# Kernel tuning notes

Hardware: AMD Instinct MI355X
Metric: run time of the kernel (lower is better)

## Reference

```python
import jax, jax.numpy as jnp
import numpy as np

B, S, E, H = 2, 2048, 2048, 16
D = E // H  # head_dim = 128


def rotate_half(x):
    x1, x2 = jnp.split(x, 2, axis=-1)
    return jnp.concatenate([-x2, x1], axis=-1)


def rope_sincos(seq_len, dim):
    inv_freq = 1.0 / (10000.0 ** (jnp.arange(0, dim, 2, dtype=jnp.float32) / dim))
    t = jnp.arange(seq_len, dtype=jnp.float32)
    freqs = jnp.outer(t, inv_freq)            # [S, D/2]
    emb = jnp.concatenate([freqs, freqs], -1)  # [S, D]
    return jnp.sin(emb), jnp.cos(emb)


def apply_rope(x, sin, cos):
    # x: [B, S, H, D]; sin/cos: [S, D] -> [1, S, 1, D]
    sin = sin[None, :, None, :]
    cos = cos[None, :, None, :]
    return x * cos + rotate_half(x) * sin


def setup_inputs() -> dict:
    key = jax.random.key(0)
    k1, k2 = jax.random.split(key)
    x = jax.random.normal(k1, (B, S, E), dtype=jnp.float32)
    # causal boolean mask [B, 1, S, S]
    mask = jnp.broadcast_to(jnp.tril(jnp.ones((S, S), dtype=bool))[None, None], (B, 1, S, S))
    # fused QKV projection weight (hk.Linear, no bias): [E, 3E]
    W_qkv = jax.random.normal(k2, (E, 3 * E), dtype=jnp.float32) / np.sqrt(E)
    return {"x": x, "mask": mask, "W_qkv": W_qkv}


def reference(x, mask, W_qkv):
    seq_len = x.shape[1]
    qkv = x @ W_qkv                               # [B, S, 3E]
    q, k, v = jnp.split(qkv, 3, axis=-1)
    q = q.reshape(-1, seq_len, H, D)
    k = k.reshape(-1, seq_len, H, D)
    v = v.reshape(-1, seq_len, H, D)
    sin, cos = rope_sincos(seq_len, D)
    q = apply_rope(q, sin, cos)
    k = apply_rope(k, sin, cos)
    attn = jnp.einsum('bqhd,bkhd->bhqk', q, k) / jnp.sqrt(jnp.float32(D))
    m = jnp.broadcast_to(mask, (mask.shape[0], H, seq_len, k.shape[1]))
    attn = jnp.where(m, attn, -jnp.inf)
    attn = jax.nn.softmax(attn, axis=-1)
    out = jnp.einsum('bhqk,bkhd->bqhd', attn, v)
    return out.reshape(-1, seq_len, H * D)
```

## Files before the change

kernel.cpp:

```cpp
#include <hip/hip_runtime.h>

typedef __bf16 bf16;
typedef __bf16 bf16x8 __attribute__((ext_vector_type(8)));
typedef __bf16 bf16x4 __attribute__((ext_vector_type(4)));
typedef float f32x4 __attribute__((ext_vector_type(4)));

#define MFMA16(a, b, c) __builtin_amdgcn_mfma_f32_16x16x32_bf16(a, b, c, 0, 0, 0)

#define Bq 2
#define Sq 2048
#define Eq 2048
#define Hq 16
#define Dq 128
#define N3E 6144

#define GLOAD_LDS16(gp, lp) \
  __builtin_amdgcn_global_load_lds( \
      (const __attribute__((address_space(1))) void*)(gp), \
      (__attribute__((address_space(3))) void*)(lp), 16, 0, 0)

__device__ __forceinline__ bf16 f2bf(float f) {
  unsigned u = __builtin_bit_cast(unsigned, f);
  u += 0x7FFFu + ((u >> 16) & 1u);
  unsigned short h = (unsigned short)(u >> 16);
  return __builtin_bit_cast(bf16, h);
}
__device__ __forceinline__ float bf2f(bf16 b) {
  unsigned short h = __builtin_bit_cast(unsigned short, b);
  return __builtin_bit_cast(float, (unsigned)h << 16);
}

__global__ __launch_bounds__(256) void convert_x(const float* __restrict__ x,
                                                 bf16* __restrict__ xb) {
  const size_t i = ((size_t)blockIdx.x * 256 + threadIdx.x) * 8;
  float4 a = *(const float4*)(x + i);
  float4 b = *(const float4*)(x + i + 4);
  bf16x8 o;
  o[0] = f2bf(a.x); o[1] = f2bf(a.y); o[2] = f2bf(a.z); o[3] = f2bf(a.w);
  o[4] = f2bf(b.x); o[5] = f2bf(b.y); o[6] = f2bf(b.z); o[7] = f2bf(b.w);
  *(bf16x8*)(xb + i) = o;
}

__global__ __launch_bounds__(256) void convert_wt(const float* __restrict__ w,
                                                  bf16* __restrict__ wt) {
  __shared__ __align__(16) bf16 T[64][72];
  const int tid = threadIdx.x;
  const int kb = blockIdx.x & 31;
  const int nb = blockIdx.x >> 5;
  const int k0 = kb * 64, n0 = nb * 64;
  {
    const int kr = tid >> 4, nc = (tid & 15) * 4;
#pragma unroll
    for (int p = 0; p < 4; ++p) {
      const int k = kr + p * 16;
      float4 v = *(const float4*)(w + (size_t)(k0 + k) * N3E + n0 + nc);
      T[nc + 0][k] = f2bf(v.x);
      T[nc + 1][k] = f2bf(v.y);
      T[nc + 2][k] = f2bf(v.z);
      T[nc + 3][k] = f2bf(v.w);
    }
  }
  __syncthreads();
#pragma unroll
  for (int q = 0; q < 2; ++q) {
    const int id = q * 256 + tid;
    const int n = id >> 3, ch = id & 7;
    bf16x8 v = *(const bf16x8*)&T[n][ch * 8];
    *(bf16x8*)(wt + (size_t)(n0 + n) * Eq + k0 + ch * 8) = v;
  }
}

__global__ __launch_bounds__(256) void rope_table(float2* __restrict__ tbl) {
  const int i = blockIdx.x * 256 + threadIdx.x;
  const int s = i >> 6, d = i & 63;
  const float freq = __expf(-(float)d * 0.14391157f);
  const float ang = (float)s * freq;
  float sv, cv;
  __sincosf(ang, &sv, &cv);
  tbl[i] = make_float2(cv, sv);
}

__global__ __launch_bounds__(512, 2) void gemm_qkv(
    const bf16* __restrict__ xb, const bf16* __restrict__ wt,
    const float2* __restrict__ tbl, bf16* __restrict__ qws,
    bf16* __restrict__ kws, bf16* __restrict__ vtws) {
  __shared__ __align__(16) bf16 LDS[3 * 24576];

  const int tid = threadIdx.x;
  const int lane = tid & 63, wv = tid >> 6;
  const int q4 = lane >> 4, c = lane & 15;
  const int wm = (wv >> 2) * 64;
  const int wn = (wv & 3) * 64;

  const int bid = blockIdx.x;
  const int wg = (bid & 7) * 96 + (bid >> 3);
  const int m0 = (wg / 24) * 128;
  const int n0 = (wg % 24) * 256;

  f32x4 acc[4][4];
#pragma unroll
  for (int i = 0; i < 4; ++i)
#pragma unroll
    for (int j = 0; j < 4; ++j) acc[i][j] = {0.f, 0.f, 0.f, 0.f};

  const int NT = Eq / 64;

  auto stage = [&](int t, int st) {
    bf16* ab = LDS + st * 24576;
    bf16* bb = ab + 8192;
    const int k0 = t * 64;
#pragma unroll
    for (int it = 0; it < 2; ++it) {
      const int slot = it * 512 + tid;
      const int row = slot >> 3, kch = slot & 7;
      const int kcs = kch ^ (row & 7);
      GLOAD_LDS16(xb + (size_t)(m0 + row) * Eq + k0 + kcs * 8, ab + slot * 8);
    }
#pragma unroll
    for (int it = 0; it < 4; ++it) {
      const int slot = it * 512 + tid;
      const int row = slot >> 3, kch = slot & 7;
      const int kcs = kch ^ (row & 7);
      GLOAD_LDS16(wt + (size_t)(n0 + row) * Eq + k0 + kcs * 8, bb + slot * 8);
    }
  };

  stage(0, 0);
  stage(1, 1);
  asm volatile("s_waitcnt vmcnt(6)" ::: "memory");
  __builtin_amdgcn_s_barrier();

  int stC = 0;
#pragma unroll 1
  for (int t = 0; t < NT; ++t) {
    if (t + 2 < NT) {
      int ss = stC + 2;
      if (ss >= 3) ss -= 3;
      stage(t + 2, ss);
    }
    const bf16* A = LDS + stC * 24576;
    const bf16* Bb = A + 8192;
#pragma unroll
    for (int kk = 0; kk < 64; kk += 32) {
      const int bch = kk >> 3;
      bf16x8 af[4], bfr[4];
#pragma unroll
      for (int i = 0; i < 4; ++i)
        af[i] = *(const bf16x8*)
            &A[(wm + i * 16 + c) * 64 + ((bch + q4) ^ (c & 7)) * 8];
#pragma unroll
      for (int j = 0; j < 4; ++j)
        bfr[j] = *(const bf16x8*)
            &Bb[(wn + j * 16 + c) * 64 + ((bch + q4) ^ (c & 7)) * 8];
      __builtin_amdgcn_s_setprio(1);
#pragma unroll
      for (int i = 0; i < 4; ++i)
#pragma unroll
        for (int j = 0; j < 4; ++j)
          acc[i][j] = MFMA16(af[i], bfr[j], acc[i][j]);
      __builtin_amdgcn_s_setprio(0);
    }
    if (t + 1 < NT) {
      if (t + 2 < NT) asm volatile("s_waitcnt vmcnt(6)" ::: "memory");
      else            asm volatile("s_waitcnt vmcnt(0)" ::: "memory");
      __builtin_amdgcn_s_barrier();
    }
    stC = stC == 2 ? 0 : stC + 1;
  }
  __syncthreads();

  const int t3 = n0 >> 11;
  const int b = m0 >> 11;
  const int s0 = m0 & 2047;
  const int h0 = (n0 & 2047) >> 7;

  bf16* E = LDS;

  if (t3 == 2) {
#pragma unroll 1
    for (int hh = 0; hh < 2; ++hh) {
      if (((wv & 3) >> 1) == hh) {
#pragma unroll
        for (int i = 0; i < 4; ++i)
#pragma unroll
          for (int j = 0; j < 4; ++j) {
            bf16x4 pv;
            pv[0] = f2bf(acc[i][j][0]); pv[1] = f2bf(acc[i][j][1]);
            pv[2] = f2bf(acc[i][j][2]); pv[3] = f2bf(acc[i][j][3]);
            *(bf16x4*)&E[((wn & 127) + j * 16 + c) * 136 + wm + i * 16 +
                         q4 * 4] = pv;
          }
      }
      __syncthreads();
      bf16* vbase = vtws + ((size_t)(b * Hq + h0 + hh) * Dq) * Sq + s0;
#pragma unroll
      for (int p = 0; p < 4; ++p) {
        const int id = p * 512 + tid;
        const int d = id >> 4, ch = id & 15;
        bf16x8 v = *(const bf16x8*)&E[d * 136 + ch * 8];
        *(bf16x8*)&vbase[(size_t)d * Sq + ch * 8] = v;
      }
      __syncthreads();
    }
  } else {
#pragma unroll 1
    for (int hh = 0; hh < 2; ++hh) {
      if (((wv & 3) >> 1) == hh) {
#pragma unroll
        for (int i = 0; i < 4; ++i)
#pragma unroll
          for (int j = 0; j < 4; ++j)
#pragma unroll
            for (int rr = 0; rr < 4; ++rr)
              E[(wm + i * 16 + q4 * 4 + rr) * 136 + (wn & 127) + j * 16 + c] =
                  f2bf(acc[i][j][rr]);
      }
      __syncthreads();
      bf16* hd = ((t3 == 0) ? qws : kws) +
                 ((size_t)(b * Hq + h0 + hh) * Sq + s0) * Dq;
#pragma unroll
      for (int p = 0; p < 2; ++p) {
        const int row = p * 64 + (tid >> 3);
        const int dlow = (tid & 7) * 8;
        const int s = s0 + row;
        bf16x8 lo = *(const bf16x8*)&E[row * 136 + dlow];
        bf16x8 hi = *(const bf16x8*)&E[row * 136 + 64 + dlow];
        const float2* tb = tbl + (size_t)s * 64 + dlow;
        bf16x8 olo, ohi;
#pragma unroll
        for (int e = 0; e < 8; ++e) {
          const float cv = tb[e].x, sv = tb[e].y;
          const float x1 = bf2f(lo[e]), x2 = bf2f(hi[e]);
          olo[e] = f2bf(x1 * cv - x2 * sv);
          ohi[e] = f2bf(x2 * cv + x1 * sv);
        }
        *(bf16x8*)&hd[(size_t)row * Dq + dlow] = olo;
        *(bf16x8*)&hd[(size_t)row * Dq + 64 + dlow] = ohi;
      }
      __syncthreads();
    }
  }
}

__global__ __launch_bounds__(256, 2) void attn_kernel(
    const bf16* __restrict__ qws, const bf16* __restrict__ kws,
    const bf16* __restrict__ vtws, float* __restrict__ out) {
  __shared__ __align__(16) bf16 Kld[2][8192];
  __shared__ __align__(16) bf16 Vld[2][8192];
  __shared__ __align__(16) bf16 Plds[4][16][72];

  const int tid = threadIdx.x, lane = tid & 63, wave = tid >> 6;
  const int q4 = lane >> 4, c = lane & 15;
  const int h = blockIdx.y, b = blockIdx.z;
  const int qt = b ? blockIdx.x : (15 - blockIdx.x);
  const size_t bh = (size_t)(b * Hq + h);
  const bf16* qbase = qws + bh * Sq * Dq;
  const bf16* kbase = kws + bh * Sq * Dq;
  const bf16* vbase = vtws + bh * Dq * Sq;
  const int q0 = qt * 128 + wave * 32;
  const float kSc = 0.08838834764831845f * 1.4426950408889634f;

  bf16x8 qf[2][4];
#pragma unroll
  for (int g = 0; g < 2; ++g)
#pragma unroll
    for (int ks = 0; ks < 4; ++ks)
      qf[g][ks] = *(const bf16x8*)
          &qbase[(size_t)(q0 + g * 16 + c) * Dq + ks * 32 + q4 * 8];

  f32x4 Ot[2][8];
  float m_i[2], l_i[2];
#pragma unroll
  for (int g = 0; g < 2; ++g) {
#pragma unroll
    for (int dj = 0; dj < 8; ++dj) Ot[g][dj] = {0.f, 0.f, 0.f, 0.f};
    m_i[g] = -1e30f; l_i[g] = 0.f;
  }

  const int nchunks = 2 * qt + 2;

#pragma unroll
  for (int it = 0; it < 4; ++it) {
    const int slot = it * 256 + tid;
    GLOAD_LDS16(kbase + (size_t)(slot & 63) * Dq + (slot >> 6) * 8,
                &Kld[0][slot * 8]);
    GLOAD_LDS16(vbase + (size_t)(slot & 127) * Sq + (slot >> 7) * 8,
                &Vld[0][slot * 8]);
  }
  __syncthreads();

  for (int kb = 0; kb < nchunks; ++kb) {
    const int buf = kb & 1;
    if (kb + 1 < nchunks) {
      const int nb = buf ^ 1;
      const int koff = (kb + 1) * 64;
#pragma unroll
      for (int it = 0; it < 4; ++it) {
        const int slot = it * 256 + tid;
        GLOAD_LDS16(kbase + (size_t)(koff + (slot & 63)) * Dq + (slot >> 6) * 8,
                    &Kld[nb][slot * 8]);
        GLOAD_LDS16(vbase + (size_t)(slot & 127) * Sq + koff + (slot >> 7) * 8,
                    &Vld[nb][slot * 8]);
      }
    }
    const bool masked = (kb >= 2 * qt);
#pragma unroll
    for (int g = 0; g < 2; ++g) {
      const int qg = q0 + g * 16 + c;
      f32x4 st[4];
#pragma unroll
      for (int j8 = 0; j8 < 4; ++j8) st[j8] = {0.f, 0.f, 0.f, 0.f};
#pragma unroll
      for (int ks = 0; ks < 4; ++ks) {
        const bf16x8 qv = qf[g][ks];
#pragma unroll
        for (int j8 = 0; j8 < 4; ++j8) {
          const bf16x8 kv = *(const bf16x8*)
              &Kld[buf][((ks * 4 + q4) * 64 + j8 * 16 + c) * 8];
          st[j8] = MFMA16(kv, qv, st[j8]);
        }
      }
      if (masked) {
        const int kb64 = kb * 64 + q4 * 4;
#pragma unroll
        for (int j8 = 0; j8 < 4; ++j8)
#pragma unroll
          for (int rr = 0; rr < 4; ++rr)
            if (kb64 + j8 * 16 + rr > qg) st[j8][rr] = -1e30f;
      }
      float mloc = -1e30f;
#pragma unroll
      for (int j8 = 0; j8 < 4; ++j8)
#pragma unroll
        for (int rr = 0; rr < 4; ++rr) mloc = fmaxf(mloc, st[j8][rr]);
      mloc = fmaxf(mloc, __shfl_xor(mloc, 16, 64));
      mloc = fmaxf(mloc, __shfl_xor(mloc, 32, 64));
      const float mn = fmaxf(m_i[g], mloc);
      const float alpha = exp2f((m_i[g] - mn) * kSc);
      m_i[g] = mn;
      float ssum = 0.f;
#pragma unroll
      for (int j8 = 0; j8 < 4; ++j8)
#pragma unroll
        for (int rr = 0; rr < 4; ++rr) {
          const float p = exp2f((st[j8][rr] - mn) * kSc);
          st[j8][rr] = p;
          ssum += p;
        }
      ssum += __shfl_xor(ssum, 16, 64);
      ssum += __shfl_xor(ssum, 32, 64);
      l_i[g] = l_i[g] * alpha + ssum;
#pragma unroll
      for (int dj = 0; dj < 8; ++dj) Ot[g][dj] *= alpha;
#pragma unroll
      for (int j8 = 0; j8 < 4; ++j8) {
        bf16x4 pk;
        pk[0] = f2bf(st[j8][0]); pk[1] = f2bf(st[j8][1]);
        pk[2] = f2bf(st[j8][2]); pk[3] = f2bf(st[j8][3]);
        *(bf16x4*)&Plds[wave][c][j8 * 16 + q4 * 4] = pk;
      }
#pragma unroll
      for (int ks = 0; ks < 2; ++ks) {
        const bf16x8 pv = *(const bf16x8*)&Plds[wave][c][ks * 32 + q4 * 8];
#pragma unroll
        for (int dj = 0; dj < 8; ++dj) {
          const bf16x8 vv = *(const bf16x8*)
              &Vld[buf][((ks * 4 + q4) * 128 + dj * 16 + c) * 8];
          Ot[g][dj] = MFMA16(vv, pv, Ot[g][dj]);
        }
      }
    }
    __syncthreads();
  }

#pragma unroll
  for (int g = 0; g < 2; ++g) {
    const float inv = 1.0f / l_i[g];
    float* orow = out + ((size_t)b * Sq + q0 + g * 16 + c) * Eq + h * Dq;
#pragma unroll
    for (int dj = 0; dj < 8; ++dj) {
      float4 o;
      o.x = Ot[g][dj][0] * inv; o.y = Ot[g][dj][1] * inv;
      o.z = Ot[g][dj][2] * inv; o.w = Ot[g][dj][3] * inv;
      *(float4*)&orow[dj * 16 + q4 * 4] = o;
    }
  }
}

extern "C" void kernel_launch(void* const* d_in, const int* in_sizes, int n_in,
                              void* d_out, int out_size, void* d_ws,
                              size_t ws_size, hipStream_t stream) {
  const float* x = (const float*)d_in[0];
  const float* w = (const float*)d_in[2];
  float* out = (float*)d_out;

  const size_t nX = (size_t)Bq * Sq * Eq;
  const size_t nW = (size_t)Eq * N3E;
  const size_t perT = (size_t)Bq * Hq * Sq * Dq;

  bf16* xb = (bf16*)d_ws;
  bf16* wt = xb + nX;
  bf16* qws = wt + nW;
  bf16* kws = qws + perT;
  bf16* vtws = kws + perT;
  float2* tbl = (float2*)(vtws + perT);

  convert_x<<<nX / (256 * 8), 256, 0, stream>>>(x, xb);
  convert_wt<<<(Eq / 64) * (N3E / 64), 256, 0, stream>>>(w, wt);
  rope_table<<<(Sq * 64) / 256, 256, 0, stream>>>(tbl);

  gemm_qkv<<<768, 512, 0, stream>>>(xb, wt, tbl, qws, kws, vtws);

  dim3 g3(Sq / 128, Hq, Bq);
  attn_kernel<<<g3, 256, 0, stream>>>(qws, kws, vtws, out);
}
```

Before: 374.1 us.

## Interleave QKV GEMM global prefetch with split MFMA phases and barriers

The QKV GEMM main loop is split into four sub-phases. Each phase loads a subset of A/B fragments from LDS, issues a slice of the next tile's global-to-LDS prefetch, then runs a small MFMA cluster between barriers, in the style of a ping-pong schedule. The goal is to spread memory issue across the compute and keep waves in lockstep so loads and MFMAs overlap better. It adds several extra barriers per iteration, which could cost throughput. The attention kernel also gains setprio around its MFMA blocks.

```diff
diff --git a/kernel.cpp b/kernel.cpp
--- a/kernel.cpp
+++ b/kernel.cpp
@@ -91,6 +91,7 @@
   const int q4 = lane >> 4, c = lane & 15;
   const int wm = (wv >> 2) * 64;
   const int wn = (wv & 3) * 64;
+  const int cx = c & 7;
 
   const int bid = blockIdx.x;
   const int wg = (bid & 7) * 96 + (bid >> 3);
@@ -105,9 +106,8 @@
 
   const int NT = Eq / 64;
 
-  auto stage = [&](int t, int st) {
+  auto stageA = [&](int t, int st) {
     bf16* ab = LDS + st * 24576;
-    bf16* bb = ab + 8192;
     const int k0 = t * 64;
 #pragma unroll
     for (int it = 0; it < 2; ++it) {
@@ -116,53 +116,96 @@
       const int kcs = kch ^ (row & 7);
       GLOAD_LDS16(xb + (size_t)(m0 + row) * Eq + k0 + kcs * 8, ab + slot * 8);
     }
-#pragma unroll
-    for (int it = 0; it < 4; ++it) {
-      const int slot = it * 512 + tid;
+  };
+  auto stageB = [&](int t, int st, int half) {
+    bf16* bb = LDS + st * 24576 + 8192;
+    const int k0 = t * 64;
+#pragma unroll
+    for (int it = 0; it < 2; ++it) {
+      const int slot = (half * 2 + it) * 512 + tid;
       const int row = slot >> 3, kch = slot & 7;
       const int kcs = kch ^ (row & 7);
       GLOAD_LDS16(wt + (size_t)(n0 + row) * Eq + k0 + kcs * 8, bb + slot * 8);
     }
   };
 
-  stage(0, 0);
-  stage(1, 1);
+  stageA(0, 0); stageB(0, 0, 0); stageB(0, 0, 1);
+  stageA(1, 1); stageB(1, 1, 0); stageB(1, 1, 1);
   asm volatile("s_waitcnt vmcnt(6)" ::: "memory");
   __builtin_amdgcn_s_barrier();
 
   int stC = 0;
 #pragma unroll 1
   for (int t = 0; t < NT; ++t) {
-    if (t + 2 < NT) {
-      int ss = stC + 2;
-      if (ss >= 3) ss -= 3;
-      stage(t + 2, ss);
-    }
     const bf16* A = LDS + stC * 24576;
     const bf16* Bb = A + 8192;
-#pragma unroll
-    for (int kk = 0; kk < 64; kk += 32) {
-      const int bch = kk >> 3;
-      bf16x8 af[4], bfr[4];
-#pragma unroll
-      for (int i = 0; i < 4; ++i)
-        af[i] = *(const bf16x8*)
-            &A[(wm + i * 16 + c) * 64 + ((bch + q4) ^ (c & 7)) * 8];
-#pragma unroll
-      for (int j = 0; j < 4; ++j)
-        bfr[j] = *(const bf16x8*)
-            &Bb[(wn + j * 16 + c) * 64 + ((bch + q4) ^ (c & 7)) * 8];
-      __builtin_amdgcn_s_setprio(1);
-#pragma unroll
-      for (int i = 0; i < 4; ++i)
-#pragma unroll
-        for (int j = 0; j < 4; ++j)
-          acc[i][j] = MFMA16(af[i], bfr[j], acc[i][j]);
-      __builtin_amdgcn_s_setprio(0);
-    }
+    int ss = stC + 2;
+    if (ss >= 3) ss -= 3;
+    const bool pf = (t + 2 < NT);
+    bf16x8 af[4], b0, b1;
+
+#pragma unroll
+    for (int i = 0; i < 4; ++i)
+      af[i] = *(const bf16x8*)&A[(wm + i * 16 + c) * 64 + (q4 ^ cx) * 8];
+    b0 = *(const bf16x8*)&Bb[(wn + 0 * 16 + c) * 64 + (q4 ^ cx) * 8];
+    b1 = *(const bf16x8*)&Bb[(wn + 1 * 16 + c) * 64 + (q4 ^ cx) * 8];
+    if (pf) stageA(t + 2, ss);
+    __builtin_amdgcn_s_barrier();
+    asm volatile("s_waitcnt lgkmcnt(0)" ::: "memory");
+    __builtin_amdgcn_s_setprio(1);
+#pragma unroll
+    for (int i = 0; i < 4; ++i) {
+      acc[i][0] = MFMA16(af[i], b0, acc[i][0]);
+      acc[i][1] = MFMA16(af[i], b1, acc[i][1]);
+    }
+    __builtin_amdgcn_s_setprio(0);
+    __builtin_amdgcn_s_barrier();
+
+    b0 = *(const bf16x8*)&Bb[(wn + 2 * 16 + c) * 64 + (q4 ^ cx) * 8];
+    b1 = *(const bf16x8*)&Bb[(wn + 3 * 16 + c) * 64 + (q4 ^ cx) * 8];
+    if (pf) stageB(t + 2, ss, 0);
+    __builtin_amdgcn_s_barrier();
+    asm volatile("s_waitcnt lgkmcnt(0)" ::: "memory");
+    __builtin_amdgcn_s_setprio(1);
+#pragma unroll
+    for (int i = 0; i < 4; ++i) {
+      acc[i][2] = MFMA16(af[i], b0, acc[i][2]);
+      acc[i][3] = MFMA16(af[i], b1, acc[i][3]);
+    }
+    __builtin_amdgcn_s_setprio(0);
+    __builtin_amdgcn_s_barrier();
+
+#pragma unroll
+    for (int i = 0; i < 4; ++i)
+      af[i] = *(const bf16x8*)&A[(wm + i * 16 + c) * 64 + ((4 + q4) ^ cx) * 8];
+    b0 = *(const bf16x8*)&Bb[(wn + 0 * 16 + c) * 64 + ((4 + q4) ^ cx) * 8];
+    b1 = *(const bf16x8*)&Bb[(wn + 1 * 16 + c) * 64 + ((4 + q4) ^ cx) * 8];
+    if (pf) stageB(t + 2, ss, 1);
+    __builtin_amdgcn_s_barrier();
+    asm volatile("s_waitcnt lgkmcnt(0)" ::: "memory");
+    __builtin_amdgcn_s_setprio(1);
+#pragma unroll
+    for (int i = 0; i < 4; ++i) {
+      acc[i][0] = MFMA16(af[i], b0, acc[i][0]);
+      acc[i][1] = MFMA16(af[i], b1, acc[i][1]);
+    }
+    __builtin_amdgcn_s_setprio(0);
+    __builtin_amdgcn_s_barrier();
+
+    b0 = *(const bf16x8*)&Bb[(wn + 2 * 16 + c) * 64 + ((4 + q4) ^ cx) * 8];
+    b1 = *(const bf16x8*)&Bb[(wn + 3 * 16 + c) * 64 + ((4 + q4) ^ cx) * 8];
+    __builtin_amdgcn_s_barrier();
+    asm volatile("s_waitcnt lgkmcnt(0)" ::: "memory");
+    __builtin_amdgcn_s_setprio(1);
+#pragma unroll
+    for (int i = 0; i < 4; ++i) {
+      acc[i][2] = MFMA16(af[i], b0, acc[i][2]);
+      acc[i][3] = MFMA16(af[i], b1, acc[i][3]);
+    }
+    __builtin_amdgcn_s_setprio(0);
     if (t + 1 < NT) {
-      if (t + 2 < NT) asm volatile("s_waitcnt vmcnt(6)" ::: "memory");
-      else            asm volatile("s_waitcnt vmcnt(0)" ::: "memory");
+      if (pf) asm volatile("s_waitcnt vmcnt(6)" ::: "memory");
+      else    asm volatile("s_waitcnt vmcnt(0)" ::: "memory");
       __builtin_amdgcn_s_barrier();
     }
     stC = stC == 2 ? 0 : stC + 1;
@@ -310,6 +353,7 @@
       f32x4 st[4];
 #pragma unroll
       for (int j8 = 0; j8 < 4; ++j8) st[j8] = {0.f, 0.f, 0.f, 0.f};
+      __builtin_amdgcn_s_setprio(1);
 #pragma unroll
       for (int ks = 0; ks < 4; ++ks) {
         const bf16x8 qv = qf[g][ks];
@@ -320,6 +364,7 @@
           st[j8] = MFMA16(kv, qv, st[j8]);
         }
       }
+      __builtin_amdgcn_s_setprio(0);
       if (masked) {
         const int kb64 = kb * 64 + q4 * 4;
 #pragma unroll
@@ -359,6 +404,7 @@
         pk[2] = f2bf(st[j8][2]); pk[3] = f2bf(st[j8][3]);
         *(bf16x4*)&Plds[wave][c][j8 * 16 + q4 * 4] = pk;
       }
+      __builtin_amdgcn_s_setprio(1);
 #pragma unroll
       for (int ks = 0; ks < 2; ++ks) {
         const bf16x8 pv = *(const bf16x8*)&Plds[wave][c][ks * 32 + q4 * 8];
@@ -369,6 +415,7 @@
           Ot[g][dj] = MFMA16(vv, pv, Ot[g][dj]);
         }
       }
+      __builtin_amdgcn_s_setprio(0);
     }
     __syncthreads();
   }
```

Result: no change. 373.7 us (-0.1%).

## Enlarge QKV GEMM tile to 256x256 with interleaved load/compute pipeline

Applied to the files above, without the earlier changes.

The QKV projection GEMM now uses a 256x256 output tile per 512-thread block, giving each wave 128x64 of output, and launches half as many blocks. The old triple-buffered LDS ring is replaced by a double buffer. Each K step is split into four quarter-tile MFMA phases, with the global-to-LDS loads for later stages issued between them and barriers plus lgkmcnt waits in between, to overlap memory traffic with matrix work and raise reuse per loaded byte. The epilogue is widened to the larger tile, and the attention kernel raises wave priority around its MFMA loops. The cost is higher register pressure from doubled accumulators, more barriers, and fewer blocks (384) for the CU count.

```diff
diff --git a/kernel.cpp b/kernel.cpp
--- a/kernel.cpp
+++ b/kernel.cpp
@@ -18,6 +18,13 @@
   __builtin_amdgcn_global_load_lds( \
       (const __attribute__((address_space(1))) void*)(gp), \
       (__attribute__((address_space(3))) void*)(lp), 16, 0, 0)
+
+#define BAR() __builtin_amdgcn_s_barrier()
+#define LGKM0() \
+  do { \
+    asm volatile("s_waitcnt lgkmcnt(0)" ::: "memory"); \
+    __builtin_amdgcn_sched_barrier(0); \
+  } while (0)
 
 __device__ __forceinline__ bf16 f2bf(float f) {
   unsigned u = __builtin_bit_cast(unsigned, f);
@@ -84,88 +91,184 @@
     const bf16* __restrict__ xb, const bf16* __restrict__ wt,
     const float2* __restrict__ tbl, bf16* __restrict__ qws,
     bf16* __restrict__ kws, bf16* __restrict__ vtws) {
-  __shared__ __align__(16) bf16 LDS[3 * 24576];
+  __shared__ __align__(16) bf16 LDS[2 * 32768];
 
   const int tid = threadIdx.x;
   const int lane = tid & 63, wv = tid >> 6;
   const int q4 = lane >> 4, c = lane & 15;
-  const int wm = (wv >> 2) * 64;
+  const int wm = (wv >> 2) * 128;
   const int wn = (wv & 3) * 64;
+  const int cx = c & 7;
 
   const int bid = blockIdx.x;
-  const int wg = (bid & 7) * 96 + (bid >> 3);
-  const int m0 = (wg / 24) * 128;
+  const int wg = (bid & 7) * 48 + (bid >> 3);
+  const int m0 = (wg / 24) * 256;
   const int n0 = (wg % 24) * 256;
 
-  f32x4 acc[4][4];
-#pragma unroll
-  for (int i = 0; i < 4; ++i)
+  f32x4 acc[8][4];
+#pragma unroll
+  for (int i = 0; i < 8; ++i)
 #pragma unroll
     for (int j = 0; j < 4; ++j) acc[i][j] = {0.f, 0.f, 0.f, 0.f};
 
   const int NT = Eq / 64;
 
-  auto stage = [&](int t, int st) {
-    bf16* ab = LDS + st * 24576;
-    bf16* bb = ab + 8192;
-    const int k0 = t * 64;
+  auto stgA = [&](int t, int half) {
+    bf16* ab = LDS + (t & 1) * 32768;
 #pragma unroll
     for (int it = 0; it < 2; ++it) {
-      const int slot = it * 512 + tid;
-      const int row = slot >> 3, kch = slot & 7;
-      const int kcs = kch ^ (row & 7);
-      GLOAD_LDS16(xb + (size_t)(m0 + row) * Eq + k0 + kcs * 8, ab + slot * 8);
-    }
-#pragma unroll
-    for (int it = 0; it < 4; ++it) {
-      const int slot = it * 512 + tid;
-      const int row = slot >> 3, kch = slot & 7;
-      const int kcs = kch ^ (row & 7);
-      GLOAD_LDS16(wt + (size_t)(n0 + row) * Eq + k0 + kcs * 8, bb + slot * 8);
+      const int sl = half * 1024 + it * 512 + tid;
+      const int row = sl >> 3, kch = sl & 7;
+      GLOAD_LDS16(
+          xb + (size_t)(m0 + row) * Eq + t * 64 + (kch ^ (row & 7)) * 8,
+          ab + sl * 8);
     }
   };
-
-  stage(0, 0);
-  stage(1, 1);
+  auto stgB = [&](int t, int half) {
+    bf16* bb = LDS + (t & 1) * 32768 + 16384;
+#pragma unroll
+    for (int it = 0; it < 2; ++it) {
+      const int sl = half * 1024 + it * 512 + tid;
+      const int row = sl >> 3, kch = sl & 7;
+      GLOAD_LDS16(
+          wt + (size_t)(n0 + row) * Eq + t * 64 + (kch ^ (row & 7)) * 8,
+          bb + sl * 8);
+    }
+  };
+  auto rdA = [&](const bf16* Ab, int ihalf, bf16x8 (&dst)[2][4]) {
+#pragma unroll
+    for (int kk = 0; kk < 2; ++kk)
+#pragma unroll
+      for (int i = 0; i < 4; ++i)
+        dst[kk][i] = *(const bf16x8*)&Ab[(wm + ihalf * 64 + i * 16 + c) * 64 +
+                                         (((kk << 2) + q4) ^ cx) * 8];
+  };
+  auto rdB = [&](const bf16* Bb, int jhalf, bf16x8 (&dst)[2][2]) {
+#pragma unroll
+    for (int kk = 0; kk < 2; ++kk)
+#pragma unroll
+      for (int j = 0; j < 2; ++j)
+        dst[kk][j] = *(const bf16x8*)&Bb[(wn + jhalf * 32 + j * 16 + c) * 64 +
+                                         (((kk << 2) + q4) ^ cx) * 8];
+  };
+
+  stgB(0, 0); stgB(0, 1); stgA(0, 0); stgA(0, 1);
+  stgB(1, 0); stgB(1, 1); stgA(1, 0);
   asm volatile("s_waitcnt vmcnt(6)" ::: "memory");
-  __builtin_amdgcn_s_barrier();
-
-  int stC = 0;
+  BAR();
+
+  const bf16* A0b = LDS;
+  const bf16* B0b = LDS + 16384;
+  const bf16* A1b = LDS + 32768;
+  const bf16* B1b = LDS + 49152;
+
 #pragma unroll 1
-  for (int t = 0; t < NT; ++t) {
-    if (t + 2 < NT) {
-      int ss = stC + 2;
-      if (ss >= 3) ss -= 3;
-      stage(t + 2, ss);
-    }
-    const bf16* A = LDS + stC * 24576;
-    const bf16* Bb = A + 8192;
-#pragma unroll
-    for (int kk = 0; kk < 64; kk += 32) {
-      const int bch = kk >> 3;
-      bf16x8 af[4], bfr[4];
-#pragma unroll
-      for (int i = 0; i < 4; ++i)
-        af[i] = *(const bf16x8*)
-            &A[(wm + i * 16 + c) * 64 + ((bch + q4) ^ (c & 7)) * 8];
-#pragma unroll
-      for (int j = 0; j < 4; ++j)
-        bfr[j] = *(const bf16x8*)
-            &Bb[(wn + j * 16 + c) * 64 + ((bch + q4) ^ (c & 7)) * 8];
-      __builtin_amdgcn_s_setprio(1);
-#pragma unroll
-      for (int i = 0; i < 4; ++i)
-#pragma unroll
-        for (int j = 0; j < 4; ++j)
-          acc[i][j] = MFMA16(af[i], bfr[j], acc[i][j]);
-      __builtin_amdgcn_s_setprio(0);
-    }
-    if (t + 1 < NT) {
-      if (t + 2 < NT) asm volatile("s_waitcnt vmcnt(6)" ::: "memory");
-      else            asm volatile("s_waitcnt vmcnt(0)" ::: "memory");
-      __builtin_amdgcn_s_barrier();
-    }
-    stC = stC == 2 ? 0 : stC + 1;
+  for (int t = 0; t < NT; t += 2) {
+    bf16x8 afr[2][4], bA[2][2], bB[2][2];
+    rdA(A0b, 0, afr); rdB(B0b, 0, bA);
+    stgA(t + 1, 1);
+    BAR(); LGKM0();
+    __builtin_amdgcn_s_setprio(1);
+#pragma unroll
+    for (int kk = 0; kk < 2; ++kk)
+#pragma unroll
+      for (int i = 0; i < 4; ++i)
+#pragma unroll
+        for (int j = 0; j < 2; ++j)
+          acc[i][j] = MFMA16(afr[kk][i], bA[kk][j], acc[i][j]);
+    __builtin_amdgcn_s_setprio(0);
+    BAR();
+    rdB(B0b, 1, bB);
+    BAR(); LGKM0();
+    __builtin_amdgcn_s_setprio(1);
+#pragma unroll
+    for (int kk = 0; kk < 2; ++kk)
+#pragma unroll
+      for (int i = 0; i < 4; ++i)
+#pragma unroll
+        for (int j = 0; j < 2; ++j)
+          acc[i][2 + j] = MFMA16(afr[kk][i], bB[kk][j], acc[i][2 + j]);
+    __builtin_amdgcn_s_setprio(0);
+    BAR();
+    rdA(A0b, 1, afr);
+    if (t + 2 < NT) stgB(t + 2, 0);
+    BAR(); LGKM0();
+    __builtin_amdgcn_s_setprio(1);
+#pragma unroll
+    for (int kk = 0; kk < 2; ++kk)
+#pragma unroll
+      for (int i = 0; i < 4; ++i)
+#pragma unroll
+        for (int j = 0; j < 2; ++j)
+          acc[4 + i][j] = MFMA16(afr[kk][i], bA[kk][j], acc[4 + i][j]);
+    __builtin_amdgcn_s_setprio(0);
+    BAR();
+    if (t + 2 < NT) { stgB(t + 2, 1); stgA(t + 2, 0); }
+    BAR(); LGKM0();
+    __builtin_amdgcn_s_setprio(1);
+#pragma unroll
+    for (int kk = 0; kk < 2; ++kk)
+#pragma unroll
+      for (int i = 0; i < 4; ++i)
+#pragma unroll
+        for (int j = 0; j < 2; ++j)
+          acc[4 + i][2 + j] = MFMA16(afr[kk][i], bB[kk][j], acc[4 + i][2 + j]);
+    __builtin_amdgcn_s_setprio(0);
+    if (t + 2 < NT) asm volatile("s_waitcnt vmcnt(6)" ::: "memory");
+    else            asm volatile("s_waitcnt vmcnt(0)" ::: "memory");
+    BAR();
+    rdA(A1b, 0, afr); rdB(B1b, 0, bA);
+    if (t + 2 < NT) stgA(t + 2, 1);
+    BAR(); LGKM0();
+    __builtin_amdgcn_s_setprio(1);
+#pragma unroll
+    for (int kk = 0; kk < 2; ++kk)
+#pragma unroll
+      for (int i = 0; i < 4; ++i)
+#pragma unroll
+        for (int j = 0; j < 2; ++j)
+          acc[i][j] = MFMA16(afr[kk][i], bA[kk][j], acc[i][j]);
+    __builtin_amdgcn_s_setprio(0);
+    BAR();
+    rdB(B1b, 1, bB);
+    BAR(); LGKM0();
+    __builtin_amdgcn_s_setprio(1);
+#pragma unroll
+    for (int kk = 0; kk < 2; ++kk)
+#pragma unroll
+      for (int i = 0; i < 4; ++i)
+#pragma unroll
+        for (int j = 0; j < 2; ++j)
+          acc[i][2 + j] = MFMA16(afr[kk][i], bB[kk][j], acc[i][2 + j]);
+    __builtin_amdgcn_s_setprio(0);
+    BAR();
+    rdA(A1b, 1, afr);
+    if (t + 3 < NT) stgB(t + 3, 0);
+    BAR(); LGKM0();
+    __builtin_amdgcn_s_setprio(1);
+#pragma unroll
+    for (int kk = 0; kk < 2; ++kk)
+#pragma unroll
+      for (int i = 0; i < 4; ++i)
+#pragma unroll
+        for (int j = 0; j < 2; ++j)
+          acc[4 + i][j] = MFMA16(afr[kk][i], bA[kk][j], acc[4 + i][j]);
+    __builtin_amdgcn_s_setprio(0);
+    BAR();
+    if (t + 3 < NT) { stgB(t + 3, 1); stgA(t + 3, 0); }
+    BAR(); LGKM0();
+    __builtin_amdgcn_s_setprio(1);
+#pragma unroll
+    for (int kk = 0; kk < 2; ++kk)
+#pragma unroll
+      for (int i = 0; i < 4; ++i)
+#pragma unroll
+        for (int j = 0; j < 2; ++j)
+          acc[4 + i][2 + j] = MFMA16(afr[kk][i], bB[kk][j], acc[4 + i][2 + j]);
+    __builtin_amdgcn_s_setprio(0);
+    if (t + 3 < NT)      asm volatile("s_waitcnt vmcnt(6)" ::: "memory");
+    else if (t + 2 < NT) asm volatile("s_waitcnt vmcnt(0)" ::: "memory");
+    BAR();
   }
   __syncthreads();
 
@@ -179,25 +282,25 @@
   if (t3 == 2) {
 #pragma unroll 1
     for (int hh = 0; hh < 2; ++hh) {
-      if (((wv & 3) >> 1) == hh) {
-#pragma unroll
-        for (int i = 0; i < 4; ++i)
+      if ((wn >> 7) == hh) {
+#pragma unroll
+        for (int i = 0; i < 8; ++i)
 #pragma unroll
           for (int j = 0; j < 4; ++j) {
             bf16x4 pv;
             pv[0] = f2bf(acc[i][j][0]); pv[1] = f2bf(acc[i][j][1]);
             pv[2] = f2bf(acc[i][j][2]); pv[3] = f2bf(acc[i][j][3]);
-            *(bf16x4*)&E[((wn & 127) + j * 16 + c) * 136 + wm + i * 16 +
+            *(bf16x4*)&E[((wn & 127) + j * 16 + c) * 264 + wm + i * 16 +
                          q4 * 4] = pv;
           }
       }
       __syncthreads();
       bf16* vbase = vtws + ((size_t)(b * Hq + h0 + hh) * Dq) * Sq + s0;
 #pragma unroll
-      for (int p = 0; p < 4; ++p) {
+      for (int p = 0; p < 8; ++p) {
         const int id = p * 512 + tid;
-        const int d = id >> 4, ch = id & 15;
-        bf16x8 v = *(const bf16x8*)&E[d * 136 + ch * 8];
+        const int d = id >> 5, ch = id & 31;
+        bf16x8 v = *(const bf16x8*)&E[d * 264 + ch * 8];
         *(bf16x8*)&vbase[(size_t)d * Sq + ch * 8] = v;
       }
       __syncthreads();
@@ -205,9 +308,9 @@
   } else {
 #pragma unroll 1
     for (int hh = 0; hh < 2; ++hh) {
-      if (((wv & 3) >> 1) == hh) {
-#pragma unroll
-        for (int i = 0; i < 4; ++i)
+      if ((wn >> 7) == hh) {
+#pragma unroll
+        for (int i = 0; i < 8; ++i)
 #pragma unroll
           for (int j = 0; j < 4; ++j)
 #pragma unroll
@@ -219,7 +322,7 @@
       bf16* hd = ((t3 == 0) ? qws : kws) +
                  ((size_t)(b * Hq + h0 + hh) * Sq + s0) * Dq;
 #pragma unroll
-      for (int p = 0; p < 2; ++p) {
+      for (int p = 0; p < 4; ++p) {
         const int row = p * 64 + (tid >> 3);
         const int dlow = (tid & 7) * 8;
         const int s = s0 + row;
@@ -310,6 +413,7 @@
       f32x4 st[4];
 #pragma unroll
       for (int j8 = 0; j8 < 4; ++j8) st[j8] = {0.f, 0.f, 0.f, 0.f};
+      __builtin_amdgcn_s_setprio(1);
 #pragma unroll
       for (int ks = 0; ks < 4; ++ks) {
         const bf16x8 qv = qf[g][ks];
@@ -320,6 +424,7 @@
           st[j8] = MFMA16(kv, qv, st[j8]);
         }
       }
+      __builtin_amdgcn_s_setprio(0);
       if (masked) {
         const int kb64 = kb * 64 + q4 * 4;
 #pragma unroll
@@ -359,6 +464,7 @@
         pk[2] = f2bf(st[j8][2]); pk[3] = f2bf(st[j8][3]);
         *(bf16x4*)&Plds[wave][c][j8 * 16 + q4 * 4] = pk;
       }
+      __builtin_amdgcn_s_setprio(1);
 #pragma unroll
       for (int ks = 0; ks < 2; ++ks) {
         const bf16x8 pv = *(const bf16x8*)&Plds[wave][c][ks * 32 + q4 * 8];
@@ -369,6 +475,7 @@
           Ot[g][dj] = MFMA16(vv, pv, Ot[g][dj]);
         }
       }
+      __builtin_amdgcn_s_setprio(0);
     }
     __syncthreads();
   }
@@ -409,7 +516,7 @@
   convert_wt<<<(Eq / 64) * (N3E / 64), 256, 0, stream>>>(w, wt);
   rope_table<<<(Sq * 64) / 256, 256, 0, stream>>>(tbl);
 
-  gemm_qkv<<<768, 512, 0, stream>>>(xb, wt, tbl, qws, kws, vtws);
+  gemm_qkv<<<384, 512, 0, stream>>>(xb, wt, tbl, qws, kws, vtws);
 
   dim3 g3(Sq / 128, Hq, Bq);
   attn_kernel<<<g3, 256, 0, stream>>>(qws, kws, vtws, out);
```

Measured after the change: 483.4 us. 29.2% more time.
